# Kernel tuning notes

Hardware: AMD Instinct MI355X
Metric: run time of the kernel (lower is better)

## Reference

```python
import jax, jax.numpy as jnp
import numpy as np

B = 16
DRUG_LEN, PROT_LEN = 64, 1200
DIM, CONV = 64, 40


def conv1d(x, w, b):
    # x: [B, C_in, L], w: [C_out, C_in, K] (torch layout), VALID padding
    y = jax.lax.conv_general_dilated(
        x, w, window_strides=(1,), padding='VALID',
        dimension_numbers=('NCH', 'OIH', 'NCH'))
    return y + b[None, :, None]


def setup_inputs() -> dict:
    key = jax.random.key(0)
    ks = jax.random.split(key, 32)
    s = 0.05
    inp = {
        'drug_tokens': jax.random.randint(ks[0], (B, DRUG_LEN), 0, 65, dtype=jnp.int32),
        'protein_tokens': jax.random.randint(ks[1], (B, PROT_LEN), 0, 26, dtype=jnp.int32),
        'drug_emb': (jax.random.normal(ks[2], (65, DIM)) * s).at[0].set(0.0),
        'prot_emb': (jax.random.normal(ks[3], (26, DIM)) * s).at[0].set(0.0),
        'dW1': jax.random.normal(ks[4], (CONV, DIM, 4)) * s,
        'db1': jax.random.normal(ks[5], (CONV,)) * s,
        'dW2': jax.random.normal(ks[6], (CONV * 2, CONV, 6)) * s,
        'db2': jax.random.normal(ks[7], (CONV * 2,)) * s,
        'dW3': jax.random.normal(ks[8], (CONV * 4, CONV * 2, 8)) * s,
        'db3': jax.random.normal(ks[9], (CONV * 4,)) * s,
        'pW1': jax.random.normal(ks[10], (CONV, DIM, 4)) * s,
        'pb1': jax.random.normal(ks[11], (CONV,)) * s,
        'pW2': jax.random.normal(ks[12], (CONV * 2, CONV, 8)) * s,
        'pb2': jax.random.normal(ks[13], (CONV * 2,)) * s,
        'pW3': jax.random.normal(ks[14], (CONV * 4, CONV * 2, 12)) * s,
        'pb3': jax.random.normal(ks[15], (CONV * 4,)) * s,
        'dattW': jax.random.normal(ks[16], (160, 160)) * s,
        'dattb': jax.random.normal(ks[17], (160,)) * s,
        'pattW': jax.random.normal(ks[18], (160, 160)) * s,
        'pattb': jax.random.normal(ks[19], (160,)) * s,
        'attW': jax.random.normal(ks[20], (160, 160)) * s,
        'attb': jax.random.normal(ks[21], (160,)) * s,
        'fc1W': jax.random.normal(ks[22], (1024, 320)) * s,
        'fc1b': jax.random.normal(ks[23], (1024,)) * s,
        'fc2W': jax.random.normal(ks[24], (1024, 1024)) * s,
        'fc2b': jax.random.normal(ks[25], (1024,)) * s,
        'fc3W': jax.random.normal(ks[26], (512, 1024)) * s,
        'fc3b': jax.random.normal(ks[27], (512,)) * s,
        'outW': jax.random.normal(ks[28], (2, 512)) * s,
        'outb': jax.random.normal(ks[29], (2,)) * s,
    }
    return inp


def reference(drug_tokens, protein_tokens, drug_emb, prot_emb,
              dW1, db1, dW2, db2, dW3, db3,
              pW1, pb1, pW2, pb2, pW3, pb3,
              dattW, dattb, pattW, pattb, attW, attb,
              fc1W, fc1b, fc2W, fc2b, fc3W, fc3b, outW, outb):
    relu = jax.nn.relu
    # Embedding lookup, then to [B, C, L]
    de = drug_emb[drug_tokens].transpose(0, 2, 1)    # [B,64,64]
    pe = prot_emb[protein_tokens].transpose(0, 2, 1)  # [B,64,1200]
    # CNN stacks
    dc = relu(conv1d(relu(conv1d(relu(conv1d(de, dW1, db1)), dW2, db2)), dW3, db3))  # [B,160,49]
    pc = relu(conv1d(relu(conv1d(relu(conv1d(pe, pW1, pb1)), pW2, pb2)), pW3, pb3))  # [B,160,1179]
    # Per-token attention projections (Linear over channel dim)
    d_att = jnp.einsum('bcd,oc->bdo', dc, dattW) + dattb   # [B,49,160]
    p_att = jnp.einsum('bcp,oc->bpo', pc, pattW) + pattb   # [B,1179,160]
    # Broadcast outer-sum + ReLU + Linear  -> [B,49,1179,160]
    A = relu(d_att[:, :, None, :] + p_att[:, None, :, :])
    A = jnp.einsum('bdpk,ok->bdpo', A, attW) + attb
    comp_atte = jax.nn.sigmoid(jnp.mean(A, axis=2)).transpose(0, 2, 1)  # [B,160,49]
    prot_atte = jax.nn.sigmoid(jnp.mean(A, axis=1)).transpose(0, 2, 1)  # [B,160,1179]
    dc = dc * 0.5 + dc * comp_atte
    pc = pc * 0.5 + pc * prot_atte
    # Global max pool over length
    dvec = jnp.max(dc, axis=2)  # [B,160]
    pvec = jnp.max(pc, axis=2)  # [B,160]
    pair = jnp.concatenate([dvec, pvec], axis=1)  # [B,320]
    # MLP head (dropout = identity at inference)
    h = jax.nn.leaky_relu(pair @ fc1W.T + fc1b, 0.01)
    h = jax.nn.leaky_relu(h @ fc2W.T + fc2b, 0.01)
    h = jax.nn.leaky_relu(h @ fc3W.T + fc3b, 0.01)
    return h @ outW.T + outb  # [B,2]
```

## Files before the change

kernel.cpp:

```cpp
#include <hip/hip_runtime.h>
#include <hip/hip_bf16.h>

typedef __hip_bfloat16 bf16;
typedef __attribute__((ext_vector_type(8))) short short8;
typedef __attribute__((ext_vector_type(4))) float floatx4;

#define NB 16


__device__ __forceinline__ float b2f(bf16 x) { return __bfloat162float(x); }
__device__ __forceinline__ float u16bf(unsigned short u) {
    return __uint_as_float(((unsigned)u) << 16);
}
__device__ __forceinline__ unsigned short f2bu(float v) {
    union { bf16 h; unsigned short u; } cv;
    cv.h = __float2bfloat16(v);
    return cv.u;
}

__global__ void sniff_kernel(const unsigned short* __restrict__ w, int* __restrict__ flag) {
    __shared__ int cnt;
    if (threadIdx.x == 0) cnt = 0;
    __syncthreads();
    int hits = 0;
    for (int s = 0; s < 4; s++) {
        unsigned short u = w[(threadIdx.x * 4 + s) * 2];
        float v = fabsf(u16bf(u));
        if (v > 1e-6f && v < 2.0f) hits++;
    }
    atomicAdd(&cnt, hits);
    __syncthreads();
    if (threadIdx.x == 0) *flag = (cnt > 512) ? 1 : 0;
}

#define NSEG 14
struct CvtJob {
    const void* src[NSEG];
    float* dst[NSEG];
    int n[NSEG];
};

__global__ void megacvt(CvtJob job, const int* __restrict__ flagp) {
    int seg = blockIdx.y;
    int i = blockIdx.x * 256 + threadIdx.x;
    if (i >= job.n[seg]) return;
    const void* s = job.src[seg];
    if (s == nullptr) { job.dst[seg][i] = 0.f; return; }
    float v = (*flagp) ? b2f(((const bf16*)s)[i]) : ((const float*)s)[i];
    job.dst[seg][i] = v;
}

#define NPK 11
struct PackJob {
    const void* src[NPK];
    bf16* dst[NPK];
    short Cout[NPK], CIN[NPK], K[NPK], coP[NPK], CIP[NPK];
};

__global__ void packN(PackJob job, const int* __restrict__ flagp) {
    int y = blockIdx.y;
    int Cout = job.Cout[y], CIN = job.CIN[y], K = job.K[y];
    int coP = job.coP[y], CIP = job.CIP[y];
    const void* src = job.src[y];
    bf16* dst = job.dst[y];
    int i = blockIdx.x * 256 + threadIdx.x;
    int total = K * coP * CIP;
    if (i >= total) return;
    int ci = i % CIP;
    int t = i / CIP;
    int co = t % coP;
    int k = t / coP;
    float v = 0.f;
    if (co < Cout && ci < CIN) {
        int s = (co * CIN + ci) * K + k;
        v = (*flagp) ? b2f(((const bf16*)src)[s]) : ((const float*)src)[s];
    }
    dst[i] = __float2bfloat16(v);
}

template <int K, int CIN, int CHUNKS, int NW>
__device__ __forceinline__ void conv_body(unsigned short* xT,
                                          const unsigned short* xb,
                                          const unsigned short* wbase,
                                          const float* __restrict__ bias,
                                          bf16* __restrict__ y,
                                          int b, int Lin, int Lout,
                                          int Cout, int coP, int l0) {
    const int CIP = CHUNKS * 32;
    const int PCI = CIP + 8;
    const int TLX = 64 + K - 1;
    for (int i = threadIdx.x; i < TLX * CIP; i += NW * 64) {
        int ci = i / TLX, l = i - ci * TLX;
        unsigned short v = 0;
        int gl = l0 + l;
        if (ci < CIN && gl < Lin) v = xb[ci * Lin + gl];
        xT[l * PCI + ci] = v;
    }
    __syncthreads();
    int lane = threadIdx.x & 63;
    int ct = threadIdx.x >> 6;
    int n = lane & 15, quad = lane >> 4;
    floatx4 acc[4];
#pragma unroll
    for (int i = 0; i < 4; i++) acc[i] = (floatx4){0.f, 0.f, 0.f, 0.f};
#pragma unroll
    for (int k = 0; k < K; k++) {
#pragma unroll
        for (int ch = 0; ch < CHUNKS; ch++) {
            short8 a = *(const short8*)(wbase +
                        ((size_t)(k * coP + ct * 16 + n)) * CIP + ch * 32 + quad * 8);
#pragma unroll
            for (int nt = 0; nt < 4; nt++) {
                short8 bb = *(const short8*)(xT + (nt * 16 + n + k) * PCI + ch * 32 + quad * 8);
                acc[nt] = __builtin_amdgcn_mfma_f32_16x16x32_bf16(a, bb, acc[nt], 0, 0, 0);
            }
        }
    }
    int m0 = quad * 4;
#pragma unroll
    for (int nt = 0; nt < 4; nt++) {
        int l = l0 + nt * 16 + n;
        if (l >= Lout) continue;
#pragma unroll
        for (int r = 0; r < 4; r++) {
            int co = ct * 16 + m0 + r;
            if (co < Cout)
                y[((size_t)b * Cout + co) * Lout + l] =
                    __float2bfloat16(fmaxf(acc[nt][r] + bias[co], 0.f));
        }
    }
}

template <int KD, int KP, int CIN, int CHUNKS, int NW>
__global__ __launch_bounds__(NW * 64) void conv_dual(const bf16* __restrict__ xd,
                                                 const bf16* __restrict__ Wpd,
                                                 const float* __restrict__ bd,
                                                 bf16* __restrict__ yd, int LinD, int LoutD,
                                                 const bf16* __restrict__ xp,
                                                 const bf16* __restrict__ Wpp,
                                                 const float* __restrict__ bp,
                                                 bf16* __restrict__ yp, int LinP, int LoutP,
                                                 int Cout, int coP) {
    const int CIP = CHUNKS * 32;
    const int PCI = CIP + 8;
    const int TLXMAX = 64 + KP - 1;
    __shared__ __align__(16) unsigned short xT[TLXMAX * PCI];
    if (blockIdx.x < 16) {
        int b = blockIdx.x;
        conv_body<KD, CIN, CHUNKS, NW>(xT, (const unsigned short*)xd + (size_t)b * CIN * LinD,
                                   (const unsigned short*)Wpd, bd, yd, b, LinD, LoutD,
                                   Cout, coP, 0);
    } else {
        int bx = blockIdx.x - 16;
        int b = bx / 19, l0 = (bx % 19) << 6;
        conv_body<KP, CIN, CHUNKS, NW>(xT, (const unsigned short*)xp + (size_t)b * CIN * LinP,
                                   (const unsigned short*)Wpp, bp, yp, b, LinP, LoutP,
                                   Cout, coP, l0);
    }
}

__global__ __launch_bounds__(256) void conv1_mfma(const int* __restrict__ dtok,
                                                  const int* __restrict__ ptok,
                                                  const bf16* __restrict__ embDB,
                                                  const bf16* __restrict__ embPB,
                                                  const bf16* __restrict__ dW1p,
                                                  const bf16* __restrict__ pW1p,
                                                  const float* __restrict__ db1f,
                                                  const float* __restrict__ pb1f,
                                                  bf16* __restrict__ d1,
                                                  bf16* __restrict__ p1) {
    const int K = 4, CIP = 64, PCI = 72, TLX = 67, coP = 48, Cout = 40;
    __shared__ __align__(16) unsigned short xT[TLX * PCI];
    __shared__ int stok[TLX];
    bool isD = blockIdx.x < 16;
    int b, l0, Lin, Lout;
    const int* tok; const unsigned short* embB; const unsigned short* Wp;
    const float* bias; bf16* y;
    if (isD) {
        b = blockIdx.x; l0 = 0; Lin = 64; Lout = 61;
        tok = dtok; embB = (const unsigned short*)embDB;
        Wp = (const unsigned short*)dW1p; bias = db1f; y = d1;
    } else {
        int bx = blockIdx.x - 16;
        b = bx / 19; l0 = (bx % 19) << 6; Lin = 1200; Lout = 1197;
        tok = ptok; embB = (const unsigned short*)embPB;
        Wp = (const unsigned short*)pW1p; bias = pb1f; y = p1;
    }
    if (threadIdx.x < TLX) {
        int l = l0 + threadIdx.x;
        stok[threadIdx.x] = (l < Lin) ? tok[b * Lin + l] : -1;
    }
    __syncthreads();
    for (int i = threadIdx.x; i < TLX * CIP; i += 256) {
        int ci = i / TLX, l = i - ci * TLX;
        int t = stok[l];
        xT[l * PCI + ci] = (t >= 0) ? embB[t * 64 + ci] : (unsigned short)0;
    }
    __syncthreads();
    int lane = threadIdx.x & 63;
    int w = threadIdx.x >> 6;
    int n = lane & 15, quad = lane >> 4;
    if (w >= 3) return;
    floatx4 acc[4];
#pragma unroll
    for (int i = 0; i < 4; i++) acc[i] = (floatx4){0.f, 0.f, 0.f, 0.f};
#pragma unroll
    for (int k = 0; k < K; k++) {
#pragma unroll
        for (int ch = 0; ch < 2; ch++) {
            short8 a = *(const short8*)(Wp +
                        ((size_t)(k * coP + w * 16 + n)) * CIP + ch * 32 + quad * 8);
#pragma unroll
            for (int nt = 0; nt < 4; nt++) {
                short8 bb = *(const short8*)(xT + (nt * 16 + n + k) * PCI + ch * 32 + quad * 8);
                acc[nt] = __builtin_amdgcn_mfma_f32_16x16x32_bf16(a, bb, acc[nt], 0, 0, 0);
            }
        }
    }
    int m0 = quad * 4;
#pragma unroll
    for (int nt = 0; nt < 4; nt++) {
        int l = l0 + nt * 16 + n;
        if (l >= Lout) continue;
#pragma unroll
        for (int r = 0; r < 4; r++) {
            int co = w * 16 + m0 + r;
            if (co < Cout)
                y[((size_t)b * Cout + co) * Lout + l] =
                    __float2bfloat16(fmaxf(acc[nt][r] + bias[co], 0.f));
        }
    }
}

__global__ __launch_bounds__(640) void att_proj_mfma(const bf16* __restrict__ dcB,
                                                     const bf16* __restrict__ pcB,
                                                     const bf16* __restrict__ dWB,
                                                     const bf16* __restrict__ pWB,
                                                     const float* __restrict__ dbF,
                                                     const float* __restrict__ pbF,
                                                     float* __restrict__ datt,
                                                     bf16* __restrict__ pattB) {
    const int PCI = 168;
    __shared__ __align__(16) unsigned short xT[64 * PCI];
    bool isD = blockIdx.x < 16;
    int b, l0, L;
    const unsigned short* xsrc; const unsigned short* W; const float* bias;
    if (isD) {
        b = blockIdx.x; l0 = 0; L = 49;
        xsrc = (const unsigned short*)dcB; W = (const unsigned short*)dWB; bias = dbF;
    } else {
        int bx = blockIdx.x - 16;
        b = bx / 19; l0 = (bx % 19) << 6; L = 1179;
        xsrc = (const unsigned short*)pcB; W = (const unsigned short*)pWB; bias = pbF;
    }
    const unsigned short* xb = xsrc + (size_t)b * 160 * L;
    for (int i = threadIdx.x; i < 160 * 64; i += 640) {
        int c = i >> 6, j = i & 63;
        int l = l0 + j;
        xT[j * PCI + c] = (l < L) ? xb[(size_t)c * L + l] : (unsigned short)0;
    }
    __syncthreads();
    int lane = threadIdx.x & 63;
    int t = threadIdx.x >> 6;
    int n = lane & 15, quad = lane >> 4;
    floatx4 acc[4];
#pragma unroll
    for (int i = 0; i < 4; i++) acc[i] = (floatx4){0.f, 0.f, 0.f, 0.f};
#pragma unroll
    for (int ch = 0; ch < 5; ch++) {
        short8 a = *(const short8*)(W + ((size_t)(t * 16 + n)) * 160 + ch * 32 + quad * 8);
#pragma unroll
        for (int nt = 0; nt < 4; nt++) {
            short8 bb = *(const short8*)(xT + (nt * 16 + n) * PCI + ch * 32 + quad * 8);
            acc[nt] = __builtin_amdgcn_mfma_f32_16x16x32_bf16(a, bb, acc[nt], 0, 0, 0);
        }
    }
    int m0 = quad * 4;
    int o0 = t * 16 + m0;
#pragma unroll
    for (int nt = 0; nt < 4; nt++) {
        int l = l0 + nt * 16 + n;
        if (l >= L) continue;
        if (isD) {
            float4 v;
            v.x = acc[nt][0] + bias[o0 + 0];
            v.y = acc[nt][1] + bias[o0 + 1];
            v.z = acc[nt][2] + bias[o0 + 2];
            v.w = acc[nt][3] + bias[o0 + 3];
            *(float4*)(datt + ((size_t)b * 49 + l) * 160 + o0) = v;
        } else {
            ushort4 u;
            u.x = f2bu(acc[nt][0] + bias[o0 + 0]);
            u.y = f2bu(acc[nt][1] + bias[o0 + 1]);
            u.z = f2bu(acc[nt][2] + bias[o0 + 2]);
            u.w = f2bu(acc[nt][3] + bias[o0 + 3]);
            *(ushort4*)((unsigned short*)pattB + ((size_t)b * 1179 + l) * 160 + o0) = u;
        }
    }
}

__global__ __launch_bounds__(640) void mean_fused(const float* __restrict__ datt,
                                                  const bf16* __restrict__ patt,
                                                  bf16* __restrict__ MpW,
                                                  float* __restrict__ Mdpart) {
    __shared__ __align__(16) unsigned short sp[37 * 160];
    int tid = threadIdx.x;
    int b = blockIdx.x >> 5;
    int pc = blockIdx.x & 31;
    int p0 = pc * 37;
    int pmax = 1179 - p0;
    if (pmax > 37) pmax = 37;
    {
        const short8* src = (const short8*)((const unsigned short*)patt +
                                            ((size_t)b * 1179 + p0) * 160);
        short8* dst = (short8*)sp;
        int n8 = (pmax * 160) >> 3;
        for (int v = tid; v < n8; v += 640) dst[v] = src[v];
    }
    int h = tid & 3;
    int k = tid >> 2;
    int d0 = h * 13;
    int nd = (h == 3) ? 10 : 13;
    const float* drow = datt + (size_t)b * 49 * 160 + k;
    float dv[13], md[13];
#pragma unroll
    for (int i = 0; i < 13; i++) {
        dv[i] = (i < nd) ? drow[(d0 + i) * 160] : -1e30f;
        md[i] = 0.f;
    }
    __syncthreads();
    unsigned short* mp = (unsigned short*)MpW + ((size_t)b * 1184 + p0) * 160 + k;
#pragma unroll 2
    for (int pi = 0; pi < pmax; pi++) {
        float pv = u16bf(sp[pi * 160 + k]);
        float s0 = 0.f, s1 = 0.f, s2 = 0.f, s3 = 0.f;
#pragma unroll
        for (int g = 0; g < 3; g++) {
            float r0 = fmaxf(dv[g * 4 + 0] + pv, 0.f);
            float r1 = fmaxf(dv[g * 4 + 1] + pv, 0.f);
            float r2 = fmaxf(dv[g * 4 + 2] + pv, 0.f);
            float r3 = fmaxf(dv[g * 4 + 3] + pv, 0.f);
            md[g * 4 + 0] += r0; s0 += r0;
            md[g * 4 + 1] += r1; s1 += r1;
            md[g * 4 + 2] += r2; s2 += r2;
            md[g * 4 + 3] += r3; s3 += r3;
        }
        {
            float r = fmaxf(dv[12] + pv, 0.f);
            md[12] += r; s0 += r;
        }
        float s = (s0 + s1) + (s2 + s3);
        s += __shfl_xor(s, 1, 64);
        s += __shfl_xor(s, 2, 64);
        if (h == 0) mp[(size_t)pi * 160] = f2bu(s * (1.f / 49.f));
    }
    float* op = Mdpart + (((size_t)b * 32 + pc) * 49) * 160 + k;
#pragma unroll
    for (int i = 0; i < 13; i++)
        if (i < nd) op[(d0 + i) * 160] = md[i];
}

__global__ __launch_bounds__(256) void md_reduce(const float* __restrict__ Mdpart,
                                                 float* __restrict__ Md) {
    int i = blockIdx.x * 256 + threadIdx.x;
    if (i >= NB * 49 * 160) return;
    int b = i / (49 * 160);
    int dk = i - b * (49 * 160);
    const float* src = Mdpart + (size_t)b * 32 * 49 * 160 + dk;
    float s0 = 0.f, s1 = 0.f, s2 = 0.f, s3 = 0.f;
#pragma unroll
    for (int pc = 0; pc < 32; pc += 4) {
        s0 += src[(size_t)(pc + 0) * 49 * 160];
        s1 += src[(size_t)(pc + 1) * 49 * 160];
        s2 += src[(size_t)(pc + 2) * 49 * 160];
        s3 += src[(size_t)(pc + 3) * 49 * 160];
    }
    Md[i] = (s0 + s1) + (s2 + s3);
}

__global__ __launch_bounds__(640) void att_sig_mfma(const float* __restrict__ Md,
                                                    const bf16* __restrict__ MpW,
                                                    const bf16* __restrict__ wattB,
                                                    const float* __restrict__ attbF,
                                                    const bf16* __restrict__ dcB,
                                                    const bf16* __restrict__ pcB,
                                                    float* __restrict__ pair) {
    const int PCI = 168;
    __shared__ __align__(16) unsigned short sM[64 * PCI];
    bool isD = blockIdx.x < 16;
    int b, p0, L, off;
    const unsigned short* conv;
    if (isD) {
        b = blockIdx.x; p0 = 0; L = 49; off = 0; conv = (const unsigned short*)dcB;
        for (int i = threadIdx.x; i < 160 * 64; i += 640) {
            int r = i / 160, k = i - r * 160;
            float v = (r < 49) ? Md[((size_t)b * 49 + r) * 160 + k] * (1.f / 1179.f) : 0.f;
            sM[r * PCI + k] = f2bu(v);
        }
    } else {
        int bx = blockIdx.x - 16;
        b = bx / 19; p0 = (bx % 19) << 6; L = 1179; off = 160;
        conv = (const unsigned short*)pcB;
        const unsigned short* mb = (const unsigned short*)MpW + (size_t)b * 1184 * 160;
        for (int i = threadIdx.x; i < 160 * 64; i += 640) {
            int r = i / 160, k = i - r * 160;
            int p = p0 + r;
            sM[r * PCI + k] = (p < 1179) ? mb[(size_t)p * 160 + k] : (unsigned short)0;
        }
    }
    __syncthreads();
    int lane = threadIdx.x & 63;
    int t = threadIdx.x >> 6;
    int n = lane & 15, quad = lane >> 4;
    floatx4 acc[4];
#pragma unroll
    for (int i = 0; i < 4; i++) acc[i] = (floatx4){0.f, 0.f, 0.f, 0.f};
    const unsigned short* W = (const unsigned short*)wattB;
#pragma unroll
    for (int ch = 0; ch < 5; ch++) {
        short8 a = *(const short8*)(W + ((size_t)(t * 16 + n)) * 160 + ch * 32 + quad * 8);
#pragma unroll
        for (int nt = 0; nt < 4; nt++) {
            short8 bb = *(const short8*)(sM + (nt * 16 + n) * PCI + ch * 32 + quad * 8);
            acc[nt] = __builtin_amdgcn_mfma_f32_16x16x32_bf16(a, bb, acc[nt], 0, 0, 0);
        }
    }
    int m0 = quad * 4;
    float vmax[4] = {0.f, 0.f, 0.f, 0.f};
#pragma unroll
    for (int nt = 0; nt < 4; nt++) {
        int p = p0 + nt * 16 + n;
#pragma unroll
        for (int r = 0; r < 4; r++) {
            int o = t * 16 + m0 + r;
            float sig = 1.f / (1.f + __expf(-(acc[nt][r] + attbF[o])));
            float v = 0.f;
            if (p < L) v = u16bf(conv[((size_t)b * 160 + o) * L + p]) * (0.5f + sig);
            vmax[r] = fmaxf(vmax[r], v);
        }
    }
#pragma unroll
    for (int m = 1; m < 16; m <<= 1) {
#pragma unroll
        for (int r = 0; r < 4; r++)
            vmax[r] = fmaxf(vmax[r], __shfl_xor(vmax[r], m, 64));
    }
    if (n == 0) {
#pragma unroll
        for (int r = 0; r < 4; r++)
            atomicMax((unsigned int*)(pair + b * 320 + off + t * 16 + m0 + r),
                      __float_as_uint(vmax[r]));
    }
}

__global__ __launch_bounds__(256) void fc_block(const float* __restrict__ in,
                                                const void* __restrict__ W,
                                                const float* __restrict__ bias,
                                                float* __restrict__ out,
                                                int IN, int OUT,
                                                const int* __restrict__ flagp) {
    int j = blockIdx.x;
    int w = threadIdx.x >> 6, li = threadIdx.x & 63;
    int nv = IN >> 2;
    const float4* i0 = (const float4*)(in + (size_t)(w * 4 + 0) * IN);
    const float4* i1 = (const float4*)(in + (size_t)(w * 4 + 1) * IN);
    const float4* i2 = (const float4*)(in + (size_t)(w * 4 + 2) * IN);
    const float4* i3 = (const float4*)(in + (size_t)(w * 4 + 3) * IN);
    float p0 = 0.f, p1 = 0.f, p2 = 0.f, p3 = 0.f;
    if (*flagp) {
        const ushort4* w4 = (const ushort4*)((const unsigned short*)W + (size_t)j * IN);
        for (int v = li; v < nv; v += 64) {
            ushort4 u = w4[v];
            float wa = u16bf(u.x), wb = u16bf(u.y), wc = u16bf(u.z), wd = u16bf(u.w);
            float4 x;
            x = i0[v]; p0 += x.x * wa + x.y * wb + x.z * wc + x.w * wd;
            x = i1[v]; p1 += x.x * wa + x.y * wb + x.z * wc + x.w * wd;
            x = i2[v]; p2 += x.x * wa + x.y * wb + x.z * wc + x.w * wd;
            x = i3[v]; p3 += x.x * wa + x.y * wb + x.z * wc + x.w * wd;
        }
    } else {
        const float4* w4 = (const float4*)((const float*)W + (size_t)j * IN);
        for (int v = li; v < nv; v += 64) {
            float4 u = w4[v];
            float4 x;
            x = i0[v]; p0 += x.x * u.x + x.y * u.y + x.z * u.z + x.w * u.w;
            x = i1[v]; p1 += x.x * u.x + x.y * u.y + x.z * u.z + x.w * u.w;
            x = i2[v]; p2 += x.x * u.x + x.y * u.y + x.z * u.z + x.w * u.w;
            x = i3[v]; p3 += x.x * u.x + x.y * u.y + x.z * u.z + x.w * u.w;
        }
    }
#pragma unroll
    for (int m = 1; m < 64; m <<= 1) {
        p0 += __shfl_xor(p0, m, 64);
        p1 += __shfl_xor(p1, m, 64);
        p2 += __shfl_xor(p2, m, 64);
        p3 += __shfl_xor(p3, m, 64);
    }
    if (li == 0) {
        float bj = bias[j];
        float o0 = p0 + bj, o1 = p1 + bj, o2 = p2 + bj, o3 = p3 + bj;
        o0 = o0 > 0.f ? o0 : 0.01f * o0;
        o1 = o1 > 0.f ? o1 : 0.01f * o1;
        o2 = o2 > 0.f ? o2 : 0.01f * o2;
        o3 = o3 > 0.f ? o3 : 0.01f * o3;
        out[(size_t)(w * 4 + 0) * OUT + j] = o0;
        out[(size_t)(w * 4 + 1) * OUT + j] = o1;
        out[(size_t)(w * 4 + 2) * OUT + j] = o2;
        out[(size_t)(w * 4 + 3) * OUT + j] = o3;
    }
}

__global__ __launch_bounds__(256) void out_block(const float* __restrict__ h,
                                                 const void* __restrict__ W,
                                                 const float* __restrict__ biasF,
                                                 void* __restrict__ out,
                                                 const int* __restrict__ flagp) {
    int j = blockIdx.x;
    int w = threadIdx.x >> 6, li = threadIdx.x & 63;
    const int IN = 512, nv = 128;
    const float4* i0 = (const float4*)(h + (size_t)(w * 4 + 0) * IN);
    const float4* i1 = (const float4*)(h + (size_t)(w * 4 + 1) * IN);
    const float4* i2 = (const float4*)(h + (size_t)(w * 4 + 2) * IN);
    const float4* i3 = (const float4*)(h + (size_t)(w * 4 + 3) * IN);
    float p0 = 0.f, p1 = 0.f, p2 = 0.f, p3 = 0.f;
    int flag = *flagp;
    if (flag) {
        const ushort4* w4 = (const ushort4*)((const unsigned short*)W + (size_t)j * IN);
        for (int v = li; v < nv; v += 64) {
            ushort4 u = w4[v];
            float wa = u16bf(u.x), wb = u16bf(u.y), wc = u16bf(u.z), wd = u16bf(u.w);
            float4 x;
            x = i0[v]; p0 += x.x * wa + x.y * wb + x.z * wc + x.w * wd;
            x = i1[v]; p1 += x.x * wa + x.y * wb + x.z * wc + x.w * wd;
            x = i2[v]; p2 += x.x * wa + x.y * wb + x.z * wc + x.w * wd;
            x = i3[v]; p3 += x.x * wa + x.y * wb + x.z * wc + x.w * wd;
        }
    } else {
        const float4* w4 = (const float4*)((const float*)W + (size_t)j * IN);
        for (int v = li; v < nv; v += 64) {
            float4 u = w4[v];
            float4 x;
            x = i0[v]; p0 += x.x * u.x + x.y * u.y + x.z * u.z + x.w * u.w;
            x = i1[v]; p1 += x.x * u.x + x.y * u.y + x.z * u.z + x.w * u.w;
            x = i2[v]; p2 += x.x * u.x + x.y * u.y + x.z * u.z + x.w * u.w;
            x = i3[v]; p3 += x.x * u.x + x.y * u.y + x.z * u.z + x.w * u.w;
        }
    }
#pragma unroll
    for (int m = 1; m < 64; m <<= 1) {
        p0 += __shfl_xor(p0, m, 64);
        p1 += __shfl_xor(p1, m, 64);
        p2 += __shfl_xor(p2, m, 64);
        p3 += __shfl_xor(p3, m, 64);
    }
    if (li == 0) {
        float bj = biasF[j];
        float o0 = p0 + bj, o1 = p1 + bj, o2 = p2 + bj, o3 = p3 + bj;
        if (flag) {
            bf16* ob = (bf16*)out;
            ob[(w * 4 + 0) * 2 + j] = __float2bfloat16(o0);
            ob[(w * 4 + 1) * 2 + j] = __float2bfloat16(o1);
            ob[(w * 4 + 2) * 2 + j] = __float2bfloat16(o2);
            ob[(w * 4 + 3) * 2 + j] = __float2bfloat16(o3);
        } else {
            float* of = (float*)out;
            of[(w * 4 + 0) * 2 + j] = o0;
            of[(w * 4 + 1) * 2 + j] = o1;
            of[(w * 4 + 2) * 2 + j] = o2;
            of[(w * 4 + 3) * 2 + j] = o3;
        }
    }
}

extern "C" void kernel_launch(void* const* d_in, const int* in_sizes, int n_in,
                              void* d_out, int out_size, void* d_ws, size_t ws_size,
                              hipStream_t stream) {
    const int* drug_tok = (const int*)d_in[0];
    const int* prot_tok = (const int*)d_in[1];
    const void* drug_emb = d_in[2];
    const void* prot_emb = d_in[3];
    const void* dW1 = d_in[4];  const void* db1 = d_in[5];
    const void* dW2 = d_in[6];  const void* db2 = d_in[7];
    const void* dW3 = d_in[8];  const void* db3 = d_in[9];
    const void* pW1 = d_in[10]; const void* pb1 = d_in[11];
    const void* pW2 = d_in[12]; const void* pb2 = d_in[13];
    const void* pW3 = d_in[14]; const void* pb3 = d_in[15];
    const void* dattW = d_in[16]; const void* dattb = d_in[17];
    const void* pattW = d_in[18]; const void* pattb = d_in[19];
    const void* attW  = d_in[20]; const void* attb  = d_in[21];
    const void* fc1W = d_in[22]; const void* fc1b = d_in[23];
    const void* fc2W = d_in[24]; const void* fc2b = d_in[25];
    const void* fc3W = d_in[26]; const void* fc3b = d_in[27];
    const void* outW = d_in[28]; const void* outb = d_in[29];

    char* base = (char*)d_ws;
    size_t cur = 0;
    auto alloc = [&](size_t bytes) -> char* {
        char* p = base + cur;
        cur = (cur + bytes + 255) & ~(size_t)255;
        return p;
    };
    int*   flag  = (int*)alloc(256);
    bf16* embDB = (bf16*)alloc(65 * 64 * 2);
    bf16* embPB = (bf16*)alloc(26 * 64 * 2);
    bf16* dW1p = (bf16*)alloc((size_t)4 * 48 * 64 * 2);
    bf16* pW1p = (bf16*)alloc((size_t)4 * 48 * 64 * 2);
    bf16* dW2p = (bf16*)alloc((size_t)6 * 128 * 64 * 2);
    bf16* dW3p = (bf16*)alloc((size_t)8 * 192 * 96 * 2);
    bf16* pW2p = (bf16*)alloc((size_t)8 * 128 * 64 * 2);
    bf16* pW3p = (bf16*)alloc((size_t)12 * 192 * 96 * 2);
    float* db1f = (float*)alloc(40 * 4);
    float* db2f = (float*)alloc(80 * 4);
    float* db3f = (float*)alloc(160 * 4);
    float* pb1f = (float*)alloc(40 * 4);
    float* pb2f = (float*)alloc(80 * 4);
    float* pb3f = (float*)alloc(160 * 4);
    float* dattbF = (float*)alloc(160 * 4);
    float* pattbF = (float*)alloc(160 * 4);
    float* attbF  = (float*)alloc(160 * 4);
    float* fc1bF = (float*)alloc(1024 * 4);
    float* fc2bF = (float*)alloc(1024 * 4);
    float* fc3bF = (float*)alloc(512 * 4);
    float* outbF = (float*)alloc(2 * 4);
    bf16* dattWB = (bf16*)alloc(25600 * 2);
    bf16* pattWB = (bf16*)alloc(25600 * 2);
    bf16* wattB  = (bf16*)alloc(25600 * 2);
    bf16* d1  = (bf16*)alloc((size_t)NB * 40 * 61 * 2);
    bf16* d2  = (bf16*)alloc((size_t)NB * 80 * 56 * 2);
    bf16* dcB = (bf16*)alloc((size_t)NB * 160 * 49 * 2);
    bf16* p1  = (bf16*)alloc((size_t)NB * 40 * 1197 * 2);
    bf16* p2  = (bf16*)alloc((size_t)NB * 80 * 1190 * 2);
    bf16* pcB = (bf16*)alloc((size_t)NB * 160 * 1179 * 2);
    float* datt  = (float*)alloc((size_t)NB * 49 * 160 * 4);
    bf16* pattB = (bf16*)alloc((size_t)NB * 1179 * 160 * 2);
    float* Md   = (float*)alloc((size_t)NB * 49 * 160 * 4);
    float* Mdpart = (float*)alloc((size_t)NB * 32 * 49 * 160 * 4);
    bf16* MpW  = (bf16*)alloc((size_t)NB * 1184 * 160 * 2);
    float* pair = (float*)alloc(NB * 320 * 4);
    float* h1 = (float*)alloc(NB * 1024 * 4);
    float* h2 = (float*)alloc(NB * 1024 * 4);
    float* h3 = (float*)alloc(NB * 512 * 4);

    sniff_kernel<<<1, 256, 0, stream>>>((const unsigned short*)fc2W, flag);

    CvtJob job;
    int si = 0;
    auto add = [&](const void* s, float* d, int n) { job.src[si] = s; job.dst[si] = d; job.n[si] = n; si++; };
    add(db1, db1f, 40); add(db2, db2f, 80); add(db3, db3f, 160);
    add(pb1, pb1f, 40); add(pb2, pb2f, 80); add(pb3, pb3f, 160);
    add(dattb, dattbF, 160); add(pattb, pattbF, 160); add(attb, attbF, 160);
    add(fc1b, fc1bF, 1024); add(fc2b, fc2bF, 1024); add(fc3b, fc3bF, 512);
    add(outb, outbF, 2);
    add(nullptr, pair, NB * 320);
    megacvt<<<dim3(20, NSEG), 256, 0, stream>>>(job, flag);

    PackJob pj;
    int pi = 0;
    auto seg = [&](const void* s, bf16* d, int Cout, int CIN, int K, int coP, int CIP) {
        pj.src[pi] = s; pj.dst[pi] = d;
        pj.Cout[pi] = Cout; pj.CIN[pi] = CIN; pj.K[pi] = K; pj.coP[pi] = coP; pj.CIP[pi] = CIP;
        pi++;
    };
    seg(dW1, dW1p, 40, 64, 4, 48, 64);
    seg(pW1, pW1p, 40, 64, 4, 48, 64);
    seg(dW2, dW2p, 80, 40, 6, 128, 64);
    seg(pW2, pW2p, 80, 40, 8, 128, 64);
    seg(dW3, dW3p, 160, 80, 8, 192, 96);
    seg(pW3, pW3p, 160, 80, 12, 192, 96);
    seg(dattW, dattWB, 160, 160, 1, 160, 160);
    seg(pattW, pattWB, 160, 160, 1, 160, 160);
    seg(attW,  wattB,  160, 160, 1, 160, 160);
    seg(drug_emb, embDB, 65, 64, 1, 65, 64);
    seg(prot_emb, embPB, 26, 64, 1, 26, 64);
    packN<<<dim3(864, NPK), 256, 0, stream>>>(pj, flag);

    conv1_mfma<<<16 + 16 * 19, 256, 0, stream>>>(drug_tok, prot_tok, embDB, embPB,
                                                 dW1p, pW1p, db1f, pb1f, d1, p1);
    conv_dual<6, 8, 40, 2, 5><<<320, 320, 0, stream>>>(
        d1, dW2p, db2f, d2, 61, 56,
        p1, pW2p, pb2f, p2, 1197, 1190, 80, 128);
    conv_dual<8, 12, 80, 3, 10><<<320, 640, 0, stream>>>(
        d2, dW3p, db3f, dcB, 56, 49,
        p2, pW3p, pb3f, pcB, 1190, 1179, 160, 192);

    att_proj_mfma<<<320, 640, 0, stream>>>(dcB, pcB, dattWB, pattWB,
                                           dattbF, pattbF, datt, pattB);

    mean_fused<<<16 * 32, 640, 0, stream>>>(datt, pattB, MpW, Mdpart);
    md_reduce<<<490, 256, 0, stream>>>(Mdpart, Md);

    att_sig_mfma<<<320, 640, 0, stream>>>(Md, MpW, wattB, attbF, dcB, pcB, pair);

    fc_block<<<1024, 256, 0, stream>>>(pair, fc1W, fc1bF, h1, 320, 1024, flag);
    fc_block<<<1024, 256, 0, stream>>>(h1, fc2W, fc2bF, h2, 1024, 1024, flag);
    fc_block<<<512, 256, 0, stream>>>(h2, fc3W, fc3bF, h3, 1024, 512, flag);
    out_block<<<2, 256, 0, stream>>>(h3, outW, outbF, d_out, flag);
}
```

Before: 239.8 us.

## Fuse conv3 with attention projection, merge prep kernels, fold md reduce

Fuses the third conv layer with the per-token attention projection, so the conv output tile stays in shared memory and feeds the projection MFMA directly instead of being re-read from global memory by a separate kernel. Also merges the bias-convert and weight-pack kernels into one launch, and folds the drug-side partial-sum reduction into the attention-sigmoid kernel. Three launches are removed, at the cost of more shared memory in the fused conv kernel and the 16 drug blocks now summing 32 partials each serially.

```diff
diff --git a/kernel.cpp b/kernel.cpp
--- a/kernel.cpp
+++ b/kernel.cpp
@@ -39,17 +39,6 @@
     float* dst[NSEG];
     int n[NSEG];
 };
-
-__global__ void megacvt(CvtJob job, const int* __restrict__ flagp) {
-    int seg = blockIdx.y;
-    int i = blockIdx.x * 256 + threadIdx.x;
-    if (i >= job.n[seg]) return;
-    const void* s = job.src[seg];
-    if (s == nullptr) { job.dst[seg][i] = 0.f; return; }
-    float v = (*flagp) ? b2f(((const bf16*)s)[i]) : ((const float*)s)[i];
-    job.dst[seg][i] = v;
-}
-
 #define NPK 11
 struct PackJob {
     const void* src[NPK];
@@ -57,25 +46,31 @@
     short Cout[NPK], CIN[NPK], K[NPK], coP[NPK], CIP[NPK];
 };
 
-__global__ void packN(PackJob job, const int* __restrict__ flagp) {
+__global__ void prep(CvtJob cj, PackJob pj, const int* __restrict__ flagp) {
     int y = blockIdx.y;
-    int Cout = job.Cout[y], CIN = job.CIN[y], K = job.K[y];
-    int coP = job.coP[y], CIP = job.CIP[y];
-    const void* src = job.src[y];
-    bf16* dst = job.dst[y];
     int i = blockIdx.x * 256 + threadIdx.x;
-    int total = K * coP * CIP;
-    if (i >= total) return;
-    int ci = i % CIP;
-    int t = i / CIP;
-    int co = t % coP;
-    int k = t / coP;
-    float v = 0.f;
-    if (co < Cout && ci < CIN) {
-        int s = (co * CIN + ci) * K + k;
-        v = (*flagp) ? b2f(((const bf16*)src)[s]) : ((const float*)src)[s];
-    }
-    dst[i] = __float2bfloat16(v);
+    if (y < NSEG) {
+        if (i >= cj.n[y]) return;
+        const void* s = cj.src[y];
+        if (s == nullptr) { cj.dst[y][i] = 0.f; return; }
+        cj.dst[y][i] = (*flagp) ? b2f(((const bf16*)s)[i]) : ((const float*)s)[i];
+    } else {
+        int p = y - NSEG;
+        int Cout = pj.Cout[p], CIN = pj.CIN[p], K = pj.K[p];
+        int coP = pj.coP[p], CIP = pj.CIP[p];
+        int total = K * coP * CIP;
+        if (i >= total) return;
+        int ci = i % CIP;
+        int t = i / CIP;
+        int co = t % coP;
+        int k = t / coP;
+        float v = 0.f;
+        if (co < Cout && ci < CIN) {
+            int s = (co * CIN + ci) * K + k;
+            v = (*flagp) ? b2f(((const bf16*)pj.src[p])[s]) : ((const float*)pj.src[p])[s];
+        }
+        pj.dst[p][i] = __float2bfloat16(v);
+    }
 }
 
 template <int K, int CIN, int CHUNKS, int NW>
@@ -156,6 +151,131 @@
         conv_body<KP, CIN, CHUNKS, NW>(xT, (const unsigned short*)xp + (size_t)b * CIN * LinP,
                                    (const unsigned short*)Wpp, bp, yp, b, LinP, LoutP,
                                    Cout, coP, l0);
+    }
+}
+
+template <int K, int CIN, int CHUNKS, int NW>
+__device__ __forceinline__ void conv_proj_phase(unsigned short* xT, unsigned short* xP,
+                                                const unsigned short* xb,
+                                                const unsigned short* wbase,
+                                                const float* __restrict__ bias,
+                                                unsigned short* __restrict__ y,
+                                                int b, int Lin, int Lout,
+                                                int Cout, int coP, int l0) {
+    const int CIP = CHUNKS * 32;
+    const int PCI = CIP + 8;
+    const int TLX = 64 + K - 1;
+    for (int i = threadIdx.x; i < TLX * CIP; i += NW * 64) {
+        int ci = i / TLX, l = i - ci * TLX;
+        unsigned short v = 0;
+        int gl = l0 + l;
+        if (ci < CIN && gl < Lin) v = xb[ci * Lin + gl];
+        xT[l * PCI + ci] = v;
+    }
+    __syncthreads();
+    int lane = threadIdx.x & 63;
+    int ct = threadIdx.x >> 6;
+    int n = lane & 15, quad = lane >> 4;
+    floatx4 acc[4];
+#pragma unroll
+    for (int i = 0; i < 4; i++) acc[i] = (floatx4){0.f, 0.f, 0.f, 0.f};
+#pragma unroll
+    for (int k = 0; k < K; k++) {
+#pragma unroll
+        for (int ch = 0; ch < CHUNKS; ch++) {
+            short8 a = *(const short8*)(wbase +
+                        ((size_t)(k * coP + ct * 16 + n)) * CIP + ch * 32 + quad * 8);
+#pragma unroll
+            for (int nt = 0; nt < 4; nt++) {
+                short8 bb = *(const short8*)(xT + (nt * 16 + n + k) * PCI + ch * 32 + quad * 8);
+                acc[nt] = __builtin_amdgcn_mfma_f32_16x16x32_bf16(a, bb, acc[nt], 0, 0, 0);
+            }
+        }
+    }
+    int m0 = quad * 4;
+#pragma unroll
+    for (int nt = 0; nt < 4; nt++) {
+        int ll = nt * 16 + n;
+        int l = l0 + ll;
+#pragma unroll
+        for (int r = 0; r < 4; r++) {
+            int co = ct * 16 + m0 + r;
+            float val = (l < Lout) ? fmaxf(acc[nt][r] + bias[co], 0.f) : 0.f;
+            unsigned short u = f2bu(val);
+            xP[ll * 168 + co] = u;
+            if (l < Lout) y[((size_t)b * Cout + co) * Lout + l] = u;
+        }
+    }
+}
+
+template <int KD, int KP, int CIN, int CHUNKS, int NW>
+__global__ __launch_bounds__(NW * 64) void conv3_proj(
+        const bf16* __restrict__ xd, const bf16* __restrict__ Wpd,
+        const float* __restrict__ bd, bf16* __restrict__ yd, int LinD, int LoutD,
+        const bf16* __restrict__ xp, const bf16* __restrict__ Wpp,
+        const float* __restrict__ bp, bf16* __restrict__ yp, int LinP, int LoutP,
+        int Cout, int coP,
+        const bf16* __restrict__ dWB, const bf16* __restrict__ pWB,
+        const float* __restrict__ dbF, const float* __restrict__ pbF,
+        float* __restrict__ datt, bf16* __restrict__ pattB) {
+    const int CIP = CHUNKS * 32;
+    const int PCI = CIP + 8;
+    const int TLXMAX = 64 + KP - 1;
+    __shared__ __align__(16) unsigned short xT[TLXMAX * PCI];
+    __shared__ __align__(16) unsigned short xP[64 * 168];
+    bool isD = blockIdx.x < 16;
+    int b, l0, L;
+    if (isD) {
+        b = blockIdx.x; l0 = 0; L = LoutD;
+        conv_proj_phase<KD, CIN, CHUNKS, NW>(xT, xP,
+            (const unsigned short*)xd + (size_t)b * CIN * LinD,
+            (const unsigned short*)Wpd, bd, (unsigned short*)yd, b, LinD, LoutD, Cout, coP, 0);
+    } else {
+        int bx = blockIdx.x - 16;
+        b = bx / 19; l0 = (bx % 19) << 6; L = LoutP;
+        conv_proj_phase<KP, CIN, CHUNKS, NW>(xT, xP,
+            (const unsigned short*)xp + (size_t)b * CIN * LinP,
+            (const unsigned short*)Wpp, bp, (unsigned short*)yp, b, LinP, LoutP, Cout, coP, l0);
+    }
+    __syncthreads();
+    int lane = threadIdx.x & 63;
+    int t = threadIdx.x >> 6;
+    int n = lane & 15, quad = lane >> 4;
+    const unsigned short* W = (const unsigned short*)(isD ? dWB : pWB);
+    const float* pbias = isD ? dbF : pbF;
+    floatx4 acc[4];
+#pragma unroll
+    for (int i = 0; i < 4; i++) acc[i] = (floatx4){0.f, 0.f, 0.f, 0.f};
+#pragma unroll
+    for (int ch = 0; ch < 5; ch++) {
+        short8 a = *(const short8*)(W + ((size_t)(t * 16 + n)) * 160 + ch * 32 + quad * 8);
+#pragma unroll
+        for (int nt = 0; nt < 4; nt++) {
+            short8 bb = *(const short8*)(xP + (nt * 16 + n) * 168 + ch * 32 + quad * 8);
+            acc[nt] = __builtin_amdgcn_mfma_f32_16x16x32_bf16(a, bb, acc[nt], 0, 0, 0);
+        }
+    }
+    int m0 = quad * 4;
+    int o0 = t * 16 + m0;
+#pragma unroll
+    for (int nt = 0; nt < 4; nt++) {
+        int l = l0 + nt * 16 + n;
+        if (l >= L) continue;
+        if (isD) {
+            float4 v;
+            v.x = acc[nt][0] + pbias[o0 + 0];
+            v.y = acc[nt][1] + pbias[o0 + 1];
+            v.z = acc[nt][2] + pbias[o0 + 2];
+            v.w = acc[nt][3] + pbias[o0 + 3];
+            *(float4*)(datt + ((size_t)b * 49 + l) * 160 + o0) = v;
+        } else {
+            ushort4 u;
+            u.x = f2bu(acc[nt][0] + pbias[o0 + 0]);
+            u.y = f2bu(acc[nt][1] + pbias[o0 + 1]);
+            u.z = f2bu(acc[nt][2] + pbias[o0 + 2]);
+            u.w = f2bu(acc[nt][3] + pbias[o0 + 3]);
+            *(ushort4*)((unsigned short*)pattB + ((size_t)b * 1179 + l) * 160 + o0) = u;
+        }
     }
 }
 
@@ -232,73 +352,6 @@
     }
 }
 
-__global__ __launch_bounds__(640) void att_proj_mfma(const bf16* __restrict__ dcB,
-                                                     const bf16* __restrict__ pcB,
-                                                     const bf16* __restrict__ dWB,
-                                                     const bf16* __restrict__ pWB,
-                                                     const float* __restrict__ dbF,
-                                                     const float* __restrict__ pbF,
-                                                     float* __restrict__ datt,
-                                                     bf16* __restrict__ pattB) {
-    const int PCI = 168;
-    __shared__ __align__(16) unsigned short xT[64 * PCI];
-    bool isD = blockIdx.x < 16;
-    int b, l0, L;
-    const unsigned short* xsrc; const unsigned short* W; const float* bias;
-    if (isD) {
-        b = blockIdx.x; l0 = 0; L = 49;
-        xsrc = (const unsigned short*)dcB; W = (const unsigned short*)dWB; bias = dbF;
-    } else {
-        int bx = blockIdx.x - 16;
-        b = bx / 19; l0 = (bx % 19) << 6; L = 1179;
-        xsrc = (const unsigned short*)pcB; W = (const unsigned short*)pWB; bias = pbF;
-    }
-    const unsigned short* xb = xsrc + (size_t)b * 160 * L;
-    for (int i = threadIdx.x; i < 160 * 64; i += 640) {
-        int c = i >> 6, j = i & 63;
-        int l = l0 + j;
-        xT[j * PCI + c] = (l < L) ? xb[(size_t)c * L + l] : (unsigned short)0;
-    }
-    __syncthreads();
-    int lane = threadIdx.x & 63;
-    int t = threadIdx.x >> 6;
-    int n = lane & 15, quad = lane >> 4;
-    floatx4 acc[4];
-#pragma unroll
-    for (int i = 0; i < 4; i++) acc[i] = (floatx4){0.f, 0.f, 0.f, 0.f};
-#pragma unroll
-    for (int ch = 0; ch < 5; ch++) {
-        short8 a = *(const short8*)(W + ((size_t)(t * 16 + n)) * 160 + ch * 32 + quad * 8);
-#pragma unroll
-        for (int nt = 0; nt < 4; nt++) {
-            short8 bb = *(const short8*)(xT + (nt * 16 + n) * PCI + ch * 32 + quad * 8);
-            acc[nt] = __builtin_amdgcn_mfma_f32_16x16x32_bf16(a, bb, acc[nt], 0, 0, 0);
-        }
-    }
-    int m0 = quad * 4;
-    int o0 = t * 16 + m0;
-#pragma unroll
-    for (int nt = 0; nt < 4; nt++) {
-        int l = l0 + nt * 16 + n;
-        if (l >= L) continue;
-        if (isD) {
-            float4 v;
-            v.x = acc[nt][0] + bias[o0 + 0];
-            v.y = acc[nt][1] + bias[o0 + 1];
-            v.z = acc[nt][2] + bias[o0 + 2];
-            v.w = acc[nt][3] + bias[o0 + 3];
-            *(float4*)(datt + ((size_t)b * 49 + l) * 160 + o0) = v;
-        } else {
-            ushort4 u;
-            u.x = f2bu(acc[nt][0] + bias[o0 + 0]);
-            u.y = f2bu(acc[nt][1] + bias[o0 + 1]);
-            u.z = f2bu(acc[nt][2] + bias[o0 + 2]);
-            u.w = f2bu(acc[nt][3] + bias[o0 + 3]);
-            *(ushort4*)((unsigned short*)pattB + ((size_t)b * 1179 + l) * 160 + o0) = u;
-        }
-    }
-}
-
 __global__ __launch_bounds__(640) void mean_fused(const float* __restrict__ datt,
                                                   const bf16* __restrict__ patt,
                                                   bf16* __restrict__ MpW,
@@ -360,25 +413,7 @@
         if (i < nd) op[(d0 + i) * 160] = md[i];
 }
 
-__global__ __launch_bounds__(256) void md_reduce(const float* __restrict__ Mdpart,
-                                                 float* __restrict__ Md) {
-    int i = blockIdx.x * 256 + threadIdx.x;
-    if (i >= NB * 49 * 160) return;
-    int b = i / (49 * 160);
-    int dk = i - b * (49 * 160);
-    const float* src = Mdpart + (size_t)b * 32 * 49 * 160 + dk;
-    float s0 = 0.f, s1 = 0.f, s2 = 0.f, s3 = 0.f;
-#pragma unroll
-    for (int pc = 0; pc < 32; pc += 4) {
-        s0 += src[(size_t)(pc + 0) * 49 * 160];
-        s1 += src[(size_t)(pc + 1) * 49 * 160];
-        s2 += src[(size_t)(pc + 2) * 49 * 160];
-        s3 += src[(size_t)(pc + 3) * 49 * 160];
-    }
-    Md[i] = (s0 + s1) + (s2 + s3);
-}
-
-__global__ __launch_bounds__(640) void att_sig_mfma(const float* __restrict__ Md,
+__global__ __launch_bounds__(640) void att_sig_mfma(const float* __restrict__ Mdpart,
                                                     const bf16* __restrict__ MpW,
                                                     const bf16* __restrict__ wattB,
                                                     const float* __restrict__ attbF,
@@ -392,9 +427,22 @@
     const unsigned short* conv;
     if (isD) {
         b = blockIdx.x; p0 = 0; L = 49; off = 0; conv = (const unsigned short*)dcB;
+        const float* mdp = Mdpart + (size_t)b * 32 * 49 * 160;
         for (int i = threadIdx.x; i < 160 * 64; i += 640) {
             int r = i / 160, k = i - r * 160;
-            float v = (r < 49) ? Md[((size_t)b * 49 + r) * 160 + k] * (1.f / 1179.f) : 0.f;
+            float v = 0.f;
+            if (r < 49) {
+                const float* src = mdp + r * 160 + k;
+                float s0 = 0.f, s1 = 0.f, s2 = 0.f, s3 = 0.f;
+#pragma unroll
+                for (int pc = 0; pc < 32; pc += 4) {
+                    s0 += src[(size_t)(pc + 0) * 7840];
+                    s1 += src[(size_t)(pc + 1) * 7840];
+                    s2 += src[(size_t)(pc + 2) * 7840];
+                    s3 += src[(size_t)(pc + 3) * 7840];
+                }
+                v = ((s0 + s1) + (s2 + s3)) * (1.f / 1179.f);
+            }
             sM[r * PCI + k] = f2bu(v);
         }
     } else {
@@ -633,7 +681,6 @@
     bf16* pcB = (bf16*)alloc((size_t)NB * 160 * 1179 * 2);
     float* datt  = (float*)alloc((size_t)NB * 49 * 160 * 4);
     bf16* pattB = (bf16*)alloc((size_t)NB * 1179 * 160 * 2);
-    float* Md   = (float*)alloc((size_t)NB * 49 * 160 * 4);
     float* Mdpart = (float*)alloc((size_t)NB * 32 * 49 * 160 * 4);
     bf16* MpW  = (bf16*)alloc((size_t)NB * 1184 * 160 * 2);
     float* pair = (float*)alloc(NB * 320 * 4);
@@ -643,17 +690,15 @@
 
     sniff_kernel<<<1, 256, 0, stream>>>((const unsigned short*)fc2W, flag);
 
-    CvtJob job;
+    CvtJob cj;
     int si = 0;
-    auto add = [&](const void* s, float* d, int n) { job.src[si] = s; job.dst[si] = d; job.n[si] = n; si++; };
+    auto add = [&](const void* s, float* d, int n) { cj.src[si] = s; cj.dst[si] = d; cj.n[si] = n; si++; };
     add(db1, db1f, 40); add(db2, db2f, 80); add(db3, db3f, 160);
     add(pb1, pb1f, 40); add(pb2, pb2f, 80); add(pb3, pb3f, 160);
     add(dattb, dattbF, 160); add(pattb, pattbF, 160); add(attb, attbF, 160);
     add(fc1b, fc1bF, 1024); add(fc2b, fc2bF, 1024); add(fc3b, fc3bF, 512);
     add(outb, outbF, 2);
     add(nullptr, pair, NB * 320);
-    megacvt<<<dim3(20, NSEG), 256, 0, stream>>>(job, flag);
-
     PackJob pj;
     int pi = 0;
     auto seg = [&](const void* s, bf16* d, int Cout, int CIN, int K, int coP, int CIP) {
@@ -672,24 +717,21 @@
     seg(attW,  wattB,  160, 160, 1, 160, 160);
     seg(drug_emb, embDB, 65, 64, 1, 65, 64);
     seg(prot_emb, embPB, 26, 64, 1, 26, 64);
-    packN<<<dim3(864, NPK), 256, 0, stream>>>(pj, flag);
+    prep<<<dim3(864, NSEG + NPK), 256, 0, stream>>>(cj, pj, flag);
 
     conv1_mfma<<<16 + 16 * 19, 256, 0, stream>>>(drug_tok, prot_tok, embDB, embPB,
                                                  dW1p, pW1p, db1f, pb1f, d1, p1);
     conv_dual<6, 8, 40, 2, 5><<<320, 320, 0, stream>>>(
         d1, dW2p, db2f, d2, 61, 56,
         p1, pW2p, pb2f, p2, 1197, 1190, 80, 128);
-    conv_dual<8, 12, 80, 3, 10><<<320, 640, 0, stream>>>(
+    conv3_proj<8, 12, 80, 3, 10><<<320, 640, 0, stream>>>(
         d2, dW3p, db3f, dcB, 56, 49,
-        p2, pW3p, pb3f, pcB, 1190, 1179, 160, 192);
-
-    att_proj_mfma<<<320, 640, 0, stream>>>(dcB, pcB, dattWB, pattWB,
-                                           dattbF, pattbF, datt, pattB);
+        p2, pW3p, pb3f, pcB, 1190, 1179, 160, 192,
+        dattWB, pattWB, dattbF, pattbF, datt, pattB);
 
     mean_fused<<<16 * 32, 640, 0, stream>>>(datt, pattB, MpW, Mdpart);
-    md_reduce<<<490, 256, 0, stream>>>(Mdpart, Md);
-
-    att_sig_mfma<<<320, 640, 0, stream>>>(Md, MpW, wattB, attbF, dcB, pcB, pair);
+
+    att_sig_mfma<<<320, 640, 0, stream>>>(Mdpart, MpW, wattB, attbF, dcB, pcB, pair);
 
     fc_block<<<1024, 256, 0, stream>>>(pair, fc1W, fc1bF, h1, 320, 1024, flag);
     fc_block<<<1024, 256, 0, stream>>>(h1, fc2W, fc2bF, h2, 1024, 1024, flag);
```

New measurement: 241.8 us. No clear change (+0.8%).
